# Kernel optimization log

Hardware: AMD Instinct MI355X
Metric: run time of the kernel (lower is better)

The kernel has to match this reference:

```python
import jax, jax.numpy as jnp
import numpy as np

HSIG_SCALE = 0.16666667  # matches MyHSigmoid's * 0.16666667

def setup_inputs() -> dict:
    key = jax.random.key(0)
    k = jax.random.split(key, 5)
    B, C, H, W, MID = 32, 256, 56, 56, 64
    return {
        "x": jax.random.normal(k[0], (B, C, H, W), dtype=jnp.float32),
        "w1": jax.random.normal(k[1], (MID, C), dtype=jnp.float32) * 0.05,
        "b1": jax.random.normal(k[2], (MID,), dtype=jnp.float32) * 0.05,
        "w2": jax.random.normal(k[3], (C, MID), dtype=jnp.float32) * 0.05,
        "b2": jax.random.normal(k[4], (C,), dtype=jnp.float32) * 0.05,
        "inject": 0, "current_epoch": 0, "counter": 0, "inject_index": 0,
    }

def reference(x, w1, b1, w2, b2, inject, current_epoch, counter, inject_index):
    # global average pool over H,W -> [B, C]
    pooled = jnp.mean(x, axis=(2, 3))
    # 1x1 conv reduce (GEMV) + ReLU
    h = jax.nn.relu(jnp.einsum('bc,mc->bm', pooled, w1) + b1)
    # 1x1 conv expand + hard-sigmoid (relu6(y+3) * 0.16666667)
    y = jnp.einsum('bm,cm->bc', h, w2) + b2
    gate = jnp.clip(y + 3.0, 0.0, 6.0) * HSIG_SCALE
    # broadcast channel gate over spatial dims
    return x * gate[:, :, None, None]
```

## Files before the change

kernel.cpp:

```cpp
#include <hip/hip_runtime.h>
#include <stdint.h>

#define BATCH 32
#define CH    256
#define MID   64
#define HW    3136
#define HWV   784

__global__ __launch_bounds__(256) void se_pool(const float4* __restrict__ x,
                                               float* __restrict__ pooled) {
    const int p = blockIdx.x;
    const float4* base = x + (size_t)p * HWV;
    const int t = threadIdx.x;

    float sum = 0.0f;
    for (int i = t; i < HWV; i += 256) {
        float4 v = base[i];
        sum += v.x + v.y + v.z + v.w;
    }
    #pragma unroll
    for (int off = 32; off > 0; off >>= 1) sum += __shfl_down(sum, off, 64);

    __shared__ float part[4];
    if ((t & 63) == 0) part[t >> 6] = sum;
    __syncthreads();
    if (t == 0) {
        float s = part[0] + part[1] + part[2] + part[3];
        pooled[p] = s * (1.0f / (float)HW);
    }
}

__global__ __launch_bounds__(256) void se_gate(const float* __restrict__ pooled,
                                               const float* __restrict__ w1,
                                               const float* __restrict__ b1,
                                               const float* __restrict__ w2,
                                               const float* __restrict__ b2,
                                               float* __restrict__ gate) {
    const int b = blockIdx.x;
    const int t = threadIdx.x;

    __shared__ float ps[CH];
    __shared__ float hs[MID];

    ps[t] = pooled[b * CH + t];
    __syncthreads();

    if (t < MID) {
        float acc = b1[t];
        const float4* wrow = (const float4*)(w1 + t * CH);
        #pragma unroll 8
        for (int i = 0; i < CH / 4; ++i) {
            float4 wv = wrow[i];
            acc += ps[i * 4 + 0] * wv.x + ps[i * 4 + 1] * wv.y +
                   ps[i * 4 + 2] * wv.z + ps[i * 4 + 3] * wv.w;
        }
        hs[t] = fmaxf(acc, 0.0f);
    }
    __syncthreads();

    float acc = b2[t];
    const float4* wrow = (const float4*)(w2 + t * MID);
    #pragma unroll
    for (int i = 0; i < MID / 4; ++i) {
        float4 wv = wrow[i];
        acc += hs[i * 4 + 0] * wv.x + hs[i * 4 + 1] * wv.y +
               hs[i * 4 + 2] * wv.z + hs[i * 4 + 3] * wv.w;
    }
    float g = fminf(fmaxf(acc + 3.0f, 0.0f), 6.0f) * 0.16666667f;
    gate[b * CH + t] = g;
}

__global__ __launch_bounds__(256) void se_scale(const float4* __restrict__ x,
                                                const float* __restrict__ gate,
                                                float4* __restrict__ out) {
    const int p = blockIdx.x;
    const float g = gate[p];
    const float4* xb = x + (size_t)p * HWV;
    float4* ob = out + (size_t)p * HWV;
    const int t = threadIdx.x;

    for (int i = t; i < HWV; i += 256) {
        float4 v = xb[i];
        float4 r;
        r.x = v.x * g; r.y = v.y * g; r.z = v.z * g; r.w = v.w * g;
        ob[i] = r;
    }
}

extern "C" void kernel_launch(void* const* d_in, const int* in_sizes, int n_in,
                              void* d_out, int out_size, void* d_ws, size_t ws_size,
                              hipStream_t stream) {
    (void)in_sizes; (void)n_in; (void)out_size; (void)ws_size;

    const float* x  = (const float*)d_in[0];
    const float* w1 = (const float*)d_in[1];
    const float* b1 = (const float*)d_in[2];
    const float* w2 = (const float*)d_in[3];
    const float* b2 = (const float*)d_in[4];

    float* pooled = (float*)d_ws;
    float* gate   = pooled + BATCH * CH;

    se_pool<<<BATCH * CH, 256, 0, stream>>>((const float4*)x, pooled);
    se_gate<<<BATCH, 256, 0, stream>>>(pooled, w1, b1, w2, b2, gate);
    se_scale<<<BATCH * CH, 256, 0, stream>>>((const float4*)x, gate, (float4*)d_out);
}
```

Before: 218.1 us.

## Fuse gate MLP into scale kernel and use nontemporal output stores

Removes the separate gate kernel and its launch: each scale block recomputes the reduce GEMV for its batch, the single expand dot product for its channel, then scales its plane. Output is written with nontemporal stores to avoid polluting cache. This adds redundant per-block GEMV work and extra barriers before the streaming loop.

```diff
diff --git a/kernel.cpp b/kernel.cpp
--- a/kernel.cpp
+++ b/kernel.cpp
@@ -7,15 +7,17 @@
 #define HW    3136
 #define HWV   784
 
-__global__ __launch_bounds__(256) void se_pool(const float4* __restrict__ x,
+typedef __attribute__((ext_vector_type(4))) float fvec4;
+
+__global__ __launch_bounds__(256) void se_pool(const fvec4* __restrict__ x,
                                                float* __restrict__ pooled) {
     const int p = blockIdx.x;
-    const float4* base = x + (size_t)p * HWV;
+    const fvec4* base = x + (size_t)p * HWV;
     const int t = threadIdx.x;
 
     float sum = 0.0f;
     for (int i = t; i < HWV; i += 256) {
-        float4 v = base[i];
+        fvec4 v = base[i];
         sum += v.x + v.y + v.z + v.w;
     }
     #pragma unroll
@@ -25,65 +27,65 @@
     if ((t & 63) == 0) part[t >> 6] = sum;
     __syncthreads();
     if (t == 0) {
-        float s = part[0] + part[1] + part[2] + part[3];
-        pooled[p] = s * (1.0f / (float)HW);
+        pooled[p] = (part[0] + part[1] + part[2] + part[3]) * (1.0f / (float)HW);
     }
 }
 
-__global__ __launch_bounds__(256) void se_gate(const float* __restrict__ pooled,
-                                               const float* __restrict__ w1,
-                                               const float* __restrict__ b1,
-                                               const float* __restrict__ w2,
-                                               const float* __restrict__ b2,
-                                               float* __restrict__ gate) {
-    const int b = blockIdx.x;
+__global__ __launch_bounds__(256) void se_gate_scale(
+    const fvec4* __restrict__ x,
+    const float* __restrict__ pooled,
+    const float* __restrict__ w1, const float* __restrict__ b1,
+    const float* __restrict__ w2, const float* __restrict__ b2,
+    fvec4* __restrict__ out) {
+    const int p = blockIdx.x;
+    const int b = p >> 8;
+    const int c = p & 255;
     const int t = threadIdx.x;
+    const int m = t & 63;
+    const int q = t >> 6;
 
     __shared__ float ps[CH];
+    __shared__ float hp[4][MID];
     __shared__ float hs[MID];
+    __shared__ float gsh;
 
     ps[t] = pooled[b * CH + t];
     __syncthreads();
 
-    if (t < MID) {
-        float acc = b1[t];
-        const float4* wrow = (const float4*)(w1 + t * CH);
-        #pragma unroll 8
-        for (int i = 0; i < CH / 4; ++i) {
-            float4 wv = wrow[i];
-            acc += ps[i * 4 + 0] * wv.x + ps[i * 4 + 1] * wv.y +
-                   ps[i * 4 + 2] * wv.z + ps[i * 4 + 3] * wv.w;
+    {
+        float acc = 0.0f;
+        const fvec4* wrow = (const fvec4*)(w1 + m * CH + q * 64);
+        const float* pq = ps + q * 64;
+        #pragma unroll
+        for (int i = 0; i < 16; ++i) {
+            fvec4 wv = wrow[i];
+            acc += pq[4 * i + 0] * wv.x + pq[4 * i + 1] * wv.y +
+                   pq[4 * i + 2] * wv.z + pq[4 * i + 3] * wv.w;
         }
-        hs[t] = fmaxf(acc, 0.0f);
+        hp[q][m] = acc;
     }
     __syncthreads();
+    if (t < MID) {
+        hs[t] = fmaxf(b1[t] + hp[0][t] + hp[1][t] + hp[2][t] + hp[3][t], 0.0f);
+    }
+    __syncthreads();
+    if (t < 64) {
+        float v = hs[t] * w2[c * MID + t];
+        #pragma unroll
+        for (int off = 32; off > 0; off >>= 1) v += __shfl_down(v, off, 64);
+        if (t == 0) {
+            gsh = fminf(fmaxf(v + b2[c] + 3.0f, 0.0f), 6.0f) * 0.16666667f;
+        }
+    }
+    __syncthreads();
+    const float g = gsh;
 
-    float acc = b2[t];
-    const float4* wrow = (const float4*)(w2 + t * MID);
-    #pragma unroll
-    for (int i = 0; i < MID / 4; ++i) {
-        float4 wv = wrow[i];
-        acc += hs[i * 4 + 0] * wv.x + hs[i * 4 + 1] * wv.y +
-               hs[i * 4 + 2] * wv.z + hs[i * 4 + 3] * wv.w;
-    }
-    float g = fminf(fmaxf(acc + 3.0f, 0.0f), 6.0f) * 0.16666667f;
-    gate[b * CH + t] = g;
-}
-
-__global__ __launch_bounds__(256) void se_scale(const float4* __restrict__ x,
-                                                const float* __restrict__ gate,
-                                                float4* __restrict__ out) {
-    const int p = blockIdx.x;
-    const float g = gate[p];
-    const float4* xb = x + (size_t)p * HWV;
-    float4* ob = out + (size_t)p * HWV;
-    const int t = threadIdx.x;
-
+    const fvec4* xb = x + (size_t)p * HWV;
+    fvec4* ob = out + (size_t)p * HWV;
     for (int i = t; i < HWV; i += 256) {
-        float4 v = xb[i];
-        float4 r;
-        r.x = v.x * g; r.y = v.y * g; r.z = v.z * g; r.w = v.w * g;
-        ob[i] = r;
+        fvec4 v = xb[i];
+        fvec4 r = { v.x * g, v.y * g, v.z * g, v.w * g };
+        __builtin_nontemporal_store(r, ob + i);
     }
 }
 
@@ -99,9 +101,8 @@
     const float* b2 = (const float*)d_in[4];
 
     float* pooled = (float*)d_ws;
-    float* gate   = pooled + BATCH * CH;
 
-    se_pool<<<BATCH * CH, 256, 0, stream>>>((const float4*)x, pooled);
-    se_gate<<<BATCH, 256, 0, stream>>>(pooled, w1, b1, w2, b2, gate);
-    se_scale<<<BATCH * CH, 256, 0, stream>>>((const float4*)x, gate, (float4*)d_out);
+    se_pool<<<BATCH * CH, 256, 0, stream>>>((const fvec4*)x, pooled);
+    se_gate_scale<<<BATCH * CH, 256, 0, stream>>>((const fvec4*)x, pooled,
+                                                  w1, b1, w2, b2, (fvec4*)d_out);
 }
```

Measured after the change: 247.0 us. 1.13x slower.
